# Kernel optimization log

Hardware: AMD Instinct MI355X
Metric: run time of the kernel (lower is better)

Reference implementation:

```python
import jax, jax.numpy as jnp
import numpy as np

B, L_SRC, H = 16, 2048, 1024


def setup_inputs() -> dict:
    key = jax.random.key(0)
    ks = jax.random.split(key, 12)
    s = 1.0 / np.sqrt(H)
    return {
        "query": jax.random.normal(ks[0], (B, 1, H), jnp.float32),
        "states": jax.random.normal(ks[1], (B, L_SRC, H), jnp.float32),
        "states_features": jax.random.normal(ks[2], (B, L_SRC, H), jnp.float32),
        "coverage": jax.random.uniform(ks[3], (B, L_SRC, 1), jnp.float32),
        "source_mask": jax.random.randint(ks[4], (B, L_SRC), 0, 2, jnp.int32),
        "is_coverage": 1,
        "Wq": jax.random.normal(ks[5], (H, H), jnp.float32) * s,
        "bq": jax.random.normal(ks[6], (H,), jnp.float32) * s,
        "Wc": jax.random.normal(ks[7], (1, H), jnp.float32) * s,
        "v": jax.random.normal(ks[8], (H, 1), jnp.float32) * s,
        "Wout": jax.random.normal(ks[9], (H, 2 * H), jnp.float32) * s,
        "bout": jax.random.normal(ks[10], (H,), jnp.float32) * s,
    }


def reference(query, states, states_features, coverage, source_mask, is_coverage,
              Wq, bq, Wc, v, Wout, bout):
    # query: (B,1,H); states/states_features: (B,L,H); coverage: (B,L,1)
    query_features = query @ Wq.T + bq                       # (B,1,H), broadcasts over L
    total = query_features + states_features                 # (B,L,H)
    if is_coverage:
        total = total + coverage @ Wc                        # Linear(1,H), no bias
    alignments = jnp.tanh(total) @ v                         # (B,L,1)
    mask = source_mask.astype(bool)[:, :, None]              # (B,L,1)
    alignments = jnp.where(mask, alignments, -jnp.inf)
    align_vectors = jax.nn.softmax(alignments, axis=1)       # softmax over L_src
    c = jnp.einsum('bls,blh->bsh', align_vectors, states)    # (B,1,H)
    concat_c = jnp.concatenate([c, query], axis=2)           # (B,1,2H)
    attn_h = concat_c @ Wout.T + bout                         # (B,1,H)
    new_coverage = coverage + align_vectors
    return attn_h, new_coverage, align_vectors
```

## Files before the change

kernel.cpp:

```cpp
#include <hip/hip_runtime.h>
#include <cfloat>

#define HD 1024
#define LS 2048
#define NB 16
#define NCH 128
#define LPER (LS / NCH)

struct f4 { float x, y, z, w; };

__device__ inline f4 ld4(const float* p) { return *reinterpret_cast<const f4*>(p); }

__device__ inline void stage16(const float* g, float* l) {
    __builtin_amdgcn_global_load_lds(
        (const __attribute__((address_space(1))) void*)g,
        (__attribute__((address_space(3))) void*)(void*)l,
        16, 0, 0);
}

__device__ inline float ftanh(float x) {
    x = fminf(10.f, fmaxf(-10.f, x));
    float t = __expf(2.f * x);
    return 1.f - 2.f * __builtin_amdgcn_rcpf(t + 1.f);
}

__device__ inline float dotTanh(const f4& s, const f4& q, const f4& wc, const f4& v, float covs) {
    return ftanh(s.x + q.x + covs * wc.x) * v.x
         + ftanh(s.y + q.y + covs * wc.y) * v.y
         + ftanh(s.z + q.z + covs * wc.z) * v.z
         + ftanh(s.w + q.w + covs * wc.w) * v.w;
}

__device__ inline float waveReduce(float v) {
    #pragma unroll
    for (int off = 32; off; off >>= 1) v += __shfl_xor(v, off, 64);
    return v;
}

__global__ void qf_kernel(const float* __restrict__ query, const float* __restrict__ Wq,
                          const float* __restrict__ bq, float* __restrict__ qf) {
    int h = blockIdx.x;
    int tid = threadIdx.x;
    int wv = tid >> 6, lane = tid & 63;
    int k0 = tid * 4;
    f4 w = ld4(Wq + (size_t)h * HD + k0);
    __shared__ float red[4][NB];
    float acc[NB];
    #pragma unroll
    for (int b = 0; b < NB; ++b) {
        f4 q = ld4(query + b * HD + k0);
        acc[b] = w.x * q.x + w.y * q.y + w.z * q.z + w.w * q.w;
    }
    #pragma unroll
    for (int b = 0; b < NB; ++b) {
        float r = waveReduce(acc[b]);
        if (lane == 0) red[wv][b] = r;
    }
    __syncthreads();
    if (tid < NB) {
        float s = red[0][tid] + red[1][tid] + red[2][tid] + red[3][tid];
        qf[tid * HD + h] = s + bq[h];
    }
}

__global__ __launch_bounds__(256) void fusedEC_kernel(
    const float* __restrict__ sf, const float* __restrict__ qf,
    const float* __restrict__ Wc, const float* __restrict__ vv,
    const float* __restrict__ coverage, const int* __restrict__ mask,
    const int* __restrict__ is_cov_p, const float* __restrict__ states,
    float* __restrict__ e_out, float* __restrict__ cpart)
{
    __shared__ float buf[LPER * HD];
    __shared__ float e_loc[LPER];
    __shared__ float ec[LPER];
    __shared__ float wq[LPER];
    __shared__ int   ridx[LPER];
    __shared__ int   snnz;

    int chunk = blockIdx.x;
    int b = blockIdx.y;
    int tid = threadIdx.x;
    int wv = tid >> 6, lane = tid & 63;
    int l4 = lane * 4;
    int base_row = b * LS + chunk * LPER;

    if (tid < 64) {
        int mk = (tid < LPER) ? mask[base_row + tid] : 0;
        unsigned long long bm = __ballot(mk != 0);
        if (tid < LPER) e_loc[tid] = -1e30f;
        if (mk != 0) {
            int pos = __popcll(bm & ((1ull << tid) - 1));
            ridx[pos] = tid;
        }
        if (tid == 0) snnz = __popcll(bm);
    }
    __syncthreads();
    int nnz = snnz;

    for (int i = wv; i < nnz; i += 4) {
        const float* src = sf + (size_t)(base_row + ridx[i]) * HD + l4;
        float* dst = &buf[i * HD];
        stage16(src,       dst);
        stage16(src + 256, dst + 256);
        stage16(src + 512, dst + 512);
        stage16(src + 768, dst + 768);
    }

    const float* qfr = qf + b * HD + l4;
    f4 q0 = ld4(qfr),      q1 = ld4(qfr + 256),      q2 = ld4(qfr + 512),      q3 = ld4(qfr + 768);
    f4 c0 = ld4(Wc + l4),  c1 = ld4(Wc + 256 + l4),  c2 = ld4(Wc + 512 + l4),  c3 = ld4(Wc + 768 + l4);
    f4 v0 = ld4(vv + l4),  v1 = ld4(vv + 256 + l4),  v2 = ld4(vv + 512 + l4),  v3 = ld4(vv + 768 + l4);
    int covflag = *is_cov_p;

    __syncthreads();

    for (int i = wv; i < nnz; i += 4) {
        int r = ridx[i];
        float covs = covflag ? coverage[base_row + r] : 0.f;
        const float* rp = &buf[i * HD + l4];
        float a = dotTanh(ld4(rp),       q0, c0, v0, covs)
                + dotTanh(ld4(rp + 256), q1, c1, v1, covs)
                + dotTanh(ld4(rp + 512), q2, c2, v2, covs)
                + dotTanh(ld4(rp + 768), q3, c3, v3, covs);
        a = waveReduce(a);
        if (lane == 0) { ec[i] = a; e_loc[r] = a; }
    }
    __syncthreads();

    for (int i = wv; i < nnz; i += 4) {
        const float* src = states + (size_t)(base_row + ridx[i]) * HD + l4;
        float* dst = &buf[i * HD];
        stage16(src,       dst);
        stage16(src + 256, dst + 256);
        stage16(src + 512, dst + 512);
        stage16(src + 768, dst + 768);
    }
    if (tid < LPER) {
        e_out[base_row + tid] = e_loc[tid];
        if (tid < nnz) wq[tid] = __expf(ec[tid]);
    }
    __syncthreads();

    int h0 = tid * 4;
    const float* bp = &buf[h0];
    float ax = 0.f, ay = 0.f, az = 0.f, aw = 0.f;
    for (int i = 0; i < nnz; i += 4) {
        int j1 = i + 1, j2 = i + 2, j3 = i + 3;
        float w0 = wq[i];
        float w1 = (j1 < nnz) ? wq[j1] : 0.f;
        float w2 = (j2 < nnz) ? wq[j2] : 0.f;
        float w3 = (j3 < nnz) ? wq[j3] : 0.f;
        int r1 = (j1 < nnz) ? j1 : 0;
        int r2 = (j2 < nnz) ? j2 : 0;
        int r3 = (j3 < nnz) ? j3 : 0;
        f4 s0 = ld4(bp + ((size_t)i  << 10));
        f4 s1 = ld4(bp + ((size_t)r1 << 10));
        f4 s2 = ld4(bp + ((size_t)r2 << 10));
        f4 s3 = ld4(bp + ((size_t)r3 << 10));
        ax = fmaf(w0, s0.x, ax); ay = fmaf(w0, s0.y, ay); az = fmaf(w0, s0.z, az); aw = fmaf(w0, s0.w, aw);
        ax = fmaf(w1, s1.x, ax); ay = fmaf(w1, s1.y, ay); az = fmaf(w1, s1.z, az); aw = fmaf(w1, s1.w, aw);
        ax = fmaf(w2, s2.x, ax); ay = fmaf(w2, s2.y, ay); az = fmaf(w2, s2.z, az); aw = fmaf(w2, s2.w, aw);
        ax = fmaf(w3, s3.x, ax); ay = fmaf(w3, s3.y, ay); az = fmaf(w3, s3.z, az); aw = fmaf(w3, s3.w, aw);
    }
    f4 o; o.x = ax; o.y = ay; o.z = az; o.w = aw;
    *reinterpret_cast<f4*>(cpart + ((size_t)(b * NCH + chunk)) * HD + h0) = o;
}

__global__ __launch_bounds__(1024) void mid_kernel(
    const float* __restrict__ e, const float* __restrict__ coverage,
    const float* __restrict__ cpart, float* __restrict__ scale,
    float* __restrict__ csum, float* __restrict__ out_align, float* __restrict__ out_newcov)
{
    __shared__ float redm[16], reds[16];
    __shared__ float red4[4][256];
    if (blockIdx.x < 16) {
        int b = blockIdx.x;
        int t = threadIdx.x;
        int wv = t >> 6, lane = t & 63;
        float v0 = e[b * LS + t];
        float v1 = e[b * LS + t + 1024];
        float mx = fmaxf(v0, v1);
        #pragma unroll
        for (int off = 32; off; off >>= 1) mx = fmaxf(mx, __shfl_xor(mx, off, 64));
        if (lane == 0) redm[wv] = mx;
        __syncthreads();
        mx = redm[0];
        #pragma unroll
        for (int i = 1; i < 16; ++i) mx = fmaxf(mx, redm[i]);
        float e0 = __expf(v0 - mx), e1 = __expf(v1 - mx);
        float s = e0 + e1;
        #pragma unroll
        for (int off = 32; off; off >>= 1) s += __shfl_xor(s, off, 64);
        if (lane == 0) reds[wv] = s;
        __syncthreads();
        s = 0.f;
        #pragma unroll
        for (int i = 0; i < 16; ++i) s += reds[i];
        float invZ = 1.f / s;
        if (t == 0) scale[b] = __expf(-mx) * invZ;
        int i0 = b * LS + t, i1 = i0 + 1024;
        float p0 = e0 * invZ, p1 = e1 * invZ;
        out_align[i0] = p0;
        out_align[i1] = p1;
        out_newcov[i0] = coverage[i0] + p0;
        out_newcov[i1] = coverage[i1] + p1;
    } else {
        int blk = blockIdx.x - 16;
        int tt = threadIdx.x & 255;
        int g = threadIdx.x >> 8;
        int elem = blk * 256 + tt;
        int b = elem >> 10, h = elem & 1023;
        const float* p = cpart + (((size_t)(b * NCH + g * 32)) << 10) + h;
        float s = 0.f;
        #pragma unroll
        for (int ch = 0; ch < 32; ++ch) s += p[(size_t)ch << 10];
        red4[g][tt] = s;
        __syncthreads();
        if (g == 0) csum[elem] = red4[0][tt] + red4[1][tt] + red4[2][tt] + red4[3][tt];
    }
}

__global__ void out_kernel(const float* __restrict__ csum, const float* __restrict__ query,
                           const float* __restrict__ Wout, const float* __restrict__ bout,
                           const float* __restrict__ scale, float* __restrict__ attn) {
    int h = blockIdx.x;
    int tid = threadIdx.x;
    int wv = tid >> 6, lane = tid & 63;
    int j0 = tid * 8;
    const float* wr = Wout + (size_t)h * (2 * HD);
    f4 w0 = ld4(wr + j0);
    f4 w1 = ld4(wr + j0 + 4);
    const float* src = (j0 < HD) ? (csum + j0) : (query + j0 - HD);
    __shared__ float red[4][NB];
    float acc[NB];
    #pragma unroll
    for (int b = 0; b < NB; ++b) {
        f4 x0 = ld4(src + b * HD);
        f4 x1 = ld4(src + b * HD + 4);
        acc[b] = w0.x * x0.x + w0.y * x0.y + w0.z * x0.z + w0.w * x0.w
               + w1.x * x1.x + w1.y * x1.y + w1.z * x1.z + w1.w * x1.w;
    }
    #pragma unroll
    for (int b = 0; b < NB; ++b) {
        float r = waveReduce(acc[b]);
        if (lane == 0) red[wv][b] = r;
    }
    __syncthreads();
    if (tid < NB) {
        float cpartial = red[0][tid] + red[1][tid];
        float qpartial = red[2][tid] + red[3][tid];
        attn[tid * HD + h] = cpartial * scale[tid] + qpartial + bout[h];
    }
}

extern "C" void kernel_launch(void* const* d_in, const int* in_sizes, int n_in,
                              void* d_out, int out_size, void* d_ws, size_t ws_size,
                              hipStream_t stream) {
    const float* query    = (const float*)d_in[0];
    const float* states   = (const float*)d_in[1];
    const float* sf       = (const float*)d_in[2];
    const float* coverage = (const float*)d_in[3];
    const int*   mask     = (const int*)d_in[4];
    const int*   is_cov   = (const int*)d_in[5];
    const float* Wq       = (const float*)d_in[6];
    const float* bq       = (const float*)d_in[7];
    const float* Wc       = (const float*)d_in[8];
    const float* v        = (const float*)d_in[9];
    const float* Wout     = (const float*)d_in[10];
    const float* bout     = (const float*)d_in[11];

    float* out      = (float*)d_out;
    float* attn     = out;
    float* newcov   = out + 16384;
    float* alignout = out + 49152;

    float* w  = (float*)d_ws;
    float* qf      = w;
    float* e       = w + 16384;
    float* cpart   = w + 49152;
    float* scale   = w + 49152 + 2097152;
    float* csum    = scale + 16;

    qf_kernel<<<dim3(HD), dim3(256), 0, stream>>>(query, Wq, bq, qf);
    fusedEC_kernel<<<dim3(NCH, NB), dim3(256), 0, stream>>>(
        sf, qf, Wc, v, coverage, mask, is_cov, states, e, cpart);
    mid_kernel<<<dim3(80), dim3(1024), 0, stream>>>(e, coverage, cpart, scale, csum, alignout, newcov);
    out_kernel<<<dim3(HD), dim3(256), 0, stream>>>(csum, query, Wout, bout, scale, attn);
}
```

Baseline: 60.59 us.

## Read score features directly into registers while staging states into LDS

The score phase no longer stages states_features through LDS. Each wave now loads its up-to-four rows of states_features straight into registers and computes four dot-tanh scores at once with a batched shuffle reduction. Meanwhile the async LDS staging of the states rows is issued first, so it overlaps with the score computation, and one barrier plus the wq buffer are removed. The exponentials are recomputed per thread in the weighted-sum loop, trading a little extra ALU work for less synchronization. It assumes LPER=16 so that four rows per wave covers the chunk.

```diff
diff --git a/kernel.cpp b/kernel.cpp
--- a/kernel.cpp
+++ b/kernel.cpp
@@ -73,7 +73,6 @@
     __shared__ float buf[LPER * HD];
     __shared__ float e_loc[LPER];
     __shared__ float ec[LPER];
-    __shared__ float wq[LPER];
     __shared__ int   ridx[LPER];
     __shared__ int   snnz;
 
@@ -98,36 +97,6 @@
     int nnz = snnz;
 
     for (int i = wv; i < nnz; i += 4) {
-        const float* src = sf + (size_t)(base_row + ridx[i]) * HD + l4;
-        float* dst = &buf[i * HD];
-        stage16(src,       dst);
-        stage16(src + 256, dst + 256);
-        stage16(src + 512, dst + 512);
-        stage16(src + 768, dst + 768);
-    }
-
-    const float* qfr = qf + b * HD + l4;
-    f4 q0 = ld4(qfr),      q1 = ld4(qfr + 256),      q2 = ld4(qfr + 512),      q3 = ld4(qfr + 768);
-    f4 c0 = ld4(Wc + l4),  c1 = ld4(Wc + 256 + l4),  c2 = ld4(Wc + 512 + l4),  c3 = ld4(Wc + 768 + l4);
-    f4 v0 = ld4(vv + l4),  v1 = ld4(vv + 256 + l4),  v2 = ld4(vv + 512 + l4),  v3 = ld4(vv + 768 + l4);
-    int covflag = *is_cov_p;
-
-    __syncthreads();
-
-    for (int i = wv; i < nnz; i += 4) {
-        int r = ridx[i];
-        float covs = covflag ? coverage[base_row + r] : 0.f;
-        const float* rp = &buf[i * HD + l4];
-        float a = dotTanh(ld4(rp),       q0, c0, v0, covs)
-                + dotTanh(ld4(rp + 256), q1, c1, v1, covs)
-                + dotTanh(ld4(rp + 512), q2, c2, v2, covs)
-                + dotTanh(ld4(rp + 768), q3, c3, v3, covs);
-        a = waveReduce(a);
-        if (lane == 0) { ec[i] = a; e_loc[r] = a; }
-    }
-    __syncthreads();
-
-    for (int i = wv; i < nnz; i += 4) {
         const float* src = states + (size_t)(base_row + ridx[i]) * HD + l4;
         float* dst = &buf[i * HD];
         stage16(src,       dst);
@@ -135,28 +104,76 @@
         stage16(src + 512, dst + 512);
         stage16(src + 768, dst + 768);
     }
-    if (tid < LPER) {
-        e_out[base_row + tid] = e_loc[tid];
-        if (tid < nnz) wq[tid] = __expf(ec[tid]);
+
+    int covflag = *is_cov_p;
+    int c0 = wv, c1 = wv + 4, c2 = wv + 8, c3 = wv + 12;
+    bool p0 = c0 < nnz, p1 = c1 < nnz, p2 = c2 < nnz, p3 = c3 < nnz;
+    int r0 = p0 ? ridx[c0] : 0;
+    int r1 = p1 ? ridx[c1] : 0;
+    int r2 = p2 ? ridx[c2] : 0;
+    int r3 = p3 ? ridx[c3] : 0;
+    float cov0 = (covflag && p0) ? coverage[base_row + r0] : 0.f;
+    float cov1 = (covflag && p1) ? coverage[base_row + r1] : 0.f;
+    float cov2 = (covflag && p2) ? coverage[base_row + r2] : 0.f;
+    float cov3 = (covflag && p3) ? coverage[base_row + r3] : 0.f;
+
+    const float* qfr = qf + b * HD + l4;
+    const float* s0p = sf + (size_t)(base_row + r0) * HD + l4;
+    const float* s1p = sf + (size_t)(base_row + r1) * HD + l4;
+    const float* s2p = sf + (size_t)(base_row + r2) * HD + l4;
+    const float* s3p = sf + (size_t)(base_row + r3) * HD + l4;
+    float a0 = 0.f, a1 = 0.f, a2 = 0.f, a3 = 0.f;
+
+    #pragma unroll
+    for (int it = 0; it < 4; ++it) {
+        int o = it * 256;
+        f4 q  = ld4(qfr + o);
+        f4 wc = ld4(Wc + o + l4);
+        f4 vf = ld4(vv + o + l4);
+        f4 s0, s1, s2, s3;
+        if (p0) s0 = ld4(s0p + o);
+        if (p1) s1 = ld4(s1p + o);
+        if (p2) s2 = ld4(s2p + o);
+        if (p3) s3 = ld4(s3p + o);
+        if (p0) a0 += dotTanh(s0, q, wc, vf, cov0);
+        if (p1) a1 += dotTanh(s1, q, wc, vf, cov1);
+        if (p2) a2 += dotTanh(s2, q, wc, vf, cov2);
+        if (p3) a3 += dotTanh(s3, q, wc, vf, cov3);
+    }
+
+    #pragma unroll
+    for (int off = 32; off; off >>= 1) {
+        a0 += __shfl_xor(a0, off, 64);
+        a1 += __shfl_xor(a1, off, 64);
+        a2 += __shfl_xor(a2, off, 64);
+        a3 += __shfl_xor(a3, off, 64);
+    }
+    if (lane == 0) {
+        if (p0) { ec[c0] = a0; e_loc[r0] = a0; }
+        if (p1) { ec[c1] = a1; e_loc[r1] = a1; }
+        if (p2) { ec[c2] = a2; e_loc[r2] = a2; }
+        if (p3) { ec[c3] = a3; e_loc[r3] = a3; }
     }
     __syncthreads();
+
+    if (tid < LPER) e_out[base_row + tid] = e_loc[tid];
 
     int h0 = tid * 4;
     const float* bp = &buf[h0];
     float ax = 0.f, ay = 0.f, az = 0.f, aw = 0.f;
     for (int i = 0; i < nnz; i += 4) {
         int j1 = i + 1, j2 = i + 2, j3 = i + 3;
-        float w0 = wq[i];
-        float w1 = (j1 < nnz) ? wq[j1] : 0.f;
-        float w2 = (j2 < nnz) ? wq[j2] : 0.f;
-        float w3 = (j3 < nnz) ? wq[j3] : 0.f;
-        int r1 = (j1 < nnz) ? j1 : 0;
-        int r2 = (j2 < nnz) ? j2 : 0;
-        int r3 = (j3 < nnz) ? j3 : 0;
+        float w0 = __expf(ec[i]);
+        float w1 = (j1 < nnz) ? __expf(ec[j1]) : 0.f;
+        float w2 = (j2 < nnz) ? __expf(ec[j2]) : 0.f;
+        float w3 = (j3 < nnz) ? __expf(ec[j3]) : 0.f;
+        int k1 = (j1 < nnz) ? j1 : 0;
+        int k2 = (j2 < nnz) ? j2 : 0;
+        int k3 = (j3 < nnz) ? j3 : 0;
         f4 s0 = ld4(bp + ((size_t)i  << 10));
-        f4 s1 = ld4(bp + ((size_t)r1 << 10));
-        f4 s2 = ld4(bp + ((size_t)r2 << 10));
-        f4 s3 = ld4(bp + ((size_t)r3 << 10));
+        f4 s1 = ld4(bp + ((size_t)k1 << 10));
+        f4 s2 = ld4(bp + ((size_t)k2 << 10));
+        f4 s3 = ld4(bp + ((size_t)k3 << 10));
         ax = fmaf(w0, s0.x, ax); ay = fmaf(w0, s0.y, ay); az = fmaf(w0, s0.z, az); aw = fmaf(w0, s0.w, aw);
         ax = fmaf(w1, s1.x, ax); ay = fmaf(w1, s1.y, ay); az = fmaf(w1, s1.z, az); aw = fmaf(w1, s1.w, aw);
         ax = fmaf(w2, s2.x, ax); ay = fmaf(w2, s2.y, ay); az = fmaf(w2, s2.z, az); aw = fmaf(w2, s2.w, aw);
```

Measured after the change: 62.42 us. +3.0%, slower.
